# Optimization experiments

Measured on AMD Instinct MI355X. Metric: run time of the kernel, lower is better.

The kernel has to match this reference:

```python
import jax, jax.numpy as jnp
import numpy as np

WH, WW = 12, 12
NUM_HEADS = 8
NW = 4


def _relative_position_index():
    ch, cw = np.meshgrid(np.arange(WH), np.arange(WW), indexing='ij')
    coords = np.stack([ch, cw]).reshape(2, -1)            # [2, Wh*Ww]
    rel = coords[:, :, None] - coords[:, None, :]         # [2, M, M]
    rel = rel.transpose(1, 2, 0)                          # [M, M, 2]
    rel[:, :, 0] += WH - 1
    rel[:, :, 1] += WW - 1
    rel[:, :, 0] *= 2 * WW - 1
    return jnp.asarray(rel.sum(-1))                       # [M, M] int


def setup_inputs() -> dict:
    key = jax.random.key(0)
    ks = jax.random.split(key, 11)
    C = 512
    B_, N = 512, WH * WW + 1
    std = 0.02
    return {
        'x': jax.random.normal(ks[0], (B_, N, C), dtype=jnp.float32),
        'mask': jnp.zeros((NW, N, N), dtype=jnp.float32),
        'rpb_table': jax.random.normal(ks[1], ((2 * WH - 1) * (2 * WW - 1), NUM_HEADS), dtype=jnp.float32) * std,
        'Wq': jax.random.normal(ks[2], (C, C), dtype=jnp.float32) * (C ** -0.5),
        'bq': jax.random.normal(ks[3], (C,), dtype=jnp.float32) * std,
        'Wk': jax.random.normal(ks[4], (C, C), dtype=jnp.float32) * (C ** -0.5),
        'bk': jax.random.normal(ks[5], (C,), dtype=jnp.float32) * std,
        'Wv': jax.random.normal(ks[6], (C, C), dtype=jnp.float32) * (C ** -0.5),
        'bv': jax.random.normal(ks[7], (C,), dtype=jnp.float32) * std,
        'Wo': jax.random.normal(ks[8], (C, C), dtype=jnp.float32) * (C ** -0.5),
        'bo': jax.random.normal(ks[9], (C,), dtype=jnp.float32) * std,
    }


def reference(x, mask, rpb_table, Wq, bq, Wk, bk, Wv, bv, Wo, bo):
    B_, N, C = x.shape
    H = NUM_HEADS
    hd = C // H
    scale = hd ** -0.5
    B = B_ // NW
    M = WH * WW  # window tokens (N = M + 1 global token)

    def proj(W, b):
        return (x @ W.T + b).reshape(B_, N, H, hd).transpose(0, 2, 1, 3)  # [B_,H,N,hd]

    q = proj(Wq, bq)
    k = proj(Wk, bk)
    v = proj(Wv, bv)

    attn = jnp.einsum('bhnd,bhmd->bhnm', q, k) * scale  # [B_,H,N,N]

    rel_idx = _relative_position_index()                 # [M,M]
    bias = rpb_table[rel_idx].transpose(2, 0, 1)          # [H,M,M]
    attn = attn.at[:, :, :M, :M].add(bias[None])          # N != M: bias on window block only

    # shifted-window mask: (nW, N, N)
    attn = (attn.reshape(B, NW, H, N, N) + mask[None, :, None]).reshape(B_, H, N, N)

    # ---- global-token attention redistribution (gx) ----
    ga = attn[:, :, -1, :].reshape(B, NW, H, N).transpose(0, 2, 1, 3)   # [B,H,NW,N]
    g1 = ga[:, :, :, :M].reshape(B, H, NW * M)                           # window keys, all windows
    g2 = ga[:, :, :, M].mean(-1, keepdims=True)                          # mean global-global logit [B,H,1]
    g = jax.nn.softmax(jnp.concatenate([g1, g2], axis=-1), axis=-1)      # [B,H,NW*M+1]
    g1 = g[:, :, :-1].reshape(B, H, NW, M).transpose(0, 2, 1, 3).reshape(B_, H, M)
    g2 = jnp.broadcast_to(g[:, :, -1][:, None, :], (B, NW, H)).reshape(B_, H, 1)
    ga_full = jnp.concatenate([g1, g2], axis=-1)[:, :, None, :]          # [B_,H,1,N]
    gx = jnp.einsum('bhqn,bhnd->bhqd', ga_full, v).transpose(0, 2, 1, 3).reshape(B_, C)
    gx = gx.reshape(B, NW, C).sum(1)                                     # sum over windows [B,C]
    gx = jnp.broadcast_to(gx[:, None, :], (B, NW, C)).reshape(B_, C)

    # ---- standard window attention ----
    attn = jax.nn.softmax(attn, axis=-1)
    out = jnp.einsum('bhnm,bhmd->bhnd', attn, v).transpose(0, 2, 1, 3).reshape(B_, N, C)
    out = out.at[:, -1, :].set(gx)
    return out @ Wo.T + bo
```

## Files before the change

kernel.cpp:

```cpp
#include <hip/hip_runtime.h>
#include <hip/hip_bf16.h>
#include <stdint.h>

#define NTOK 145
#define MTOK 144
#define CDIM 512
#define NHEAD 8
#define HD 64
#define NWIN 4
#define BWIN 512
#define MROWS (BWIN*NTOK)

typedef short short8 __attribute__((ext_vector_type(8)));
typedef float f32x4 __attribute__((ext_vector_type(4)));

__device__ __forceinline__ uint16_t f2bf(float f) {
  union { float f; uint32_t u; } x; x.f = f;
  uint32_t r = x.u + 0x7FFFu + ((x.u >> 16) & 1u);
  return (uint16_t)(r >> 16);
}
__device__ __forceinline__ float bf2f(uint16_t u) {
  union { uint32_t u; float f; } x; x.u = ((uint32_t)u) << 16; return x.f;
}
__device__ __forceinline__ uint32_t pack2(float a, float b) {
  return (uint32_t)f2bf(a) | ((uint32_t)f2bf(b) << 16);
}

#define GLL(gp, lp) __builtin_amdgcn_global_load_lds( \
    (const __attribute__((address_space(1))) uint32_t*)(gp), \
    (__attribute__((address_space(3))) uint32_t*)(lp), 16, 0, 0)

__global__ __launch_bounds__(256) void cast_x(const float* __restrict__ x,
                                              uint16_t* __restrict__ xb) {
  size_t id = ((size_t)blockIdx.x*256 + threadIdx.x)*8;
  float4 a = *(const float4*)(x+id), c = *(const float4*)(x+id+4);
  uint4 o = make_uint4(pack2(a.x,a.y), pack2(a.z,a.w), pack2(c.x,c.y), pack2(c.z,c.w));
  *(uint4*)(xb+id) = o;
}

__global__ void prep_kernel(const float* __restrict__ rpb,
                            const float* __restrict__ Wq, const float* __restrict__ bq,
                            const float* __restrict__ Wk, const float* __restrict__ bk,
                            const float* __restrict__ Wv, const float* __restrict__ bv,
                            const float* __restrict__ Wo,
                            uint16_t* __restrict__ wqkv, uint16_t* __restrict__ wo,
                            float* __restrict__ bqkv, float* __restrict__ biastab) {
  int id = blockIdx.x * 256 + threadIdx.x;
  const int A = 1536*512, B = 512*512, C2 = 1536, D = 8*144*144;
  if (id < A) {
    int n = id >> 9, k = id & 511;
    const float* W = (n < 512) ? Wq : (n < 1024) ? Wk : Wv;
    wqkv[id] = f2bf(W[(size_t)(n & 511)*512 + k]);
  } else if ((id -= A) < B) {
    wo[id] = f2bf(Wo[id]);
  } else if ((id -= B) < C2) {
    bqkv[id] = (id < 512) ? bq[id] : (id < 1024) ? bk[id-512] : bv[id-1024];
  } else if ((id -= C2) < D) {
    int h = id / (144*144); int rr = id % (144*144);
    int i = rr / 144, j = rr % 144;
    int rel = (i/12 - j/12 + 11) * 23 + (i%12 - j%12 + 11);
    biastab[id] = rpb[rel*8 + h];
  }
}

__global__ __launch_bounds__(256) void gemm_qkv(
    const uint16_t* __restrict__ xb, const uint16_t* __restrict__ wqkv,
    const float* __restrict__ bqkv,
    uint16_t* __restrict__ qb, uint16_t* __restrict__ kb, uint16_t* __restrict__ vb) {
  __shared__ __align__(16) uint16_t As[128*32];
  __shared__ __align__(16) uint16_t Bs[128*32];
  int bid = blockIdx.x;
  int mb, nb;
  if (bid < 6912) { int g = bid / 96, r = bid % 96; mb = g*8 + (r & 7); nb = r >> 3; }
  else           { int r = bid - 6912;              mb = 576 + (r & 3); nb = r >> 2; }
  int tid = threadIdx.x;
  int lane = tid & 63, w = tid >> 6;
  int wm = w >> 1, wn = w & 1;
  int lm = lane & 15, lq = lane >> 4;

  int srow = lane >> 2, scol = (lane & 3) * 8;
  const uint16_t* agp = xb   + (size_t)(mb*128 + w*32 + srow)*512 + scol;
  const uint16_t* bgp = wqkv + (size_t)(nb*128 + w*32 + srow)*512 + scol;
  uint16_t* Asw = &As[w*32*32];
  uint16_t* Bsw = &Bs[w*32*32];

  f32x4 acc[4][4];
#pragma unroll
  for (int a = 0; a < 4; a++)
#pragma unroll
    for (int b = 0; b < 4; b++) acc[a][b] = (f32x4){0.f,0.f,0.f,0.f};

  for (int kt = 0; kt < 16; kt++) {
    GLL(agp + kt*32,          Asw);
    GLL(agp + kt*32 + 16*512, Asw + 16*32);
    GLL(bgp + kt*32,          Bsw);
    GLL(bgp + kt*32 + 16*512, Bsw + 16*32);
    __syncthreads();
    short8 a[4], b[4];
#pragma unroll
    for (int t = 0; t < 4; t++) a[t] = *(short8*)&As[(wm*64 + t*16 + lm)*32 + lq*8];
#pragma unroll
    for (int t = 0; t < 4; t++) b[t] = *(short8*)&Bs[(wn*64 + t*16 + lm)*32 + lq*8];
#pragma unroll
    for (int tm = 0; tm < 4; tm++)
#pragma unroll
      for (int tn = 0; tn < 4; tn++)
        acc[tm][tn] = __builtin_amdgcn_mfma_f32_16x16x32_bf16(a[tm], b[tn], acc[tm][tn], 0, 0, 0);
    __syncthreads();
  }
#pragma unroll
  for (int tn = 0; tn < 4; tn++) {
    int n = nb*128 + wn*64 + tn*16 + lm;
    float bias = bqkv[n];
    int which = n >> 9, c = n & 511;
    uint16_t* dst = (which == 0) ? qb : (which == 1) ? kb : vb;
    int hh = c >> 6, dd = c & 63;
#pragma unroll
    for (int tm = 0; tm < 4; tm++) {
#pragma unroll
      for (int r = 0; r < 4; r++) {
        int m = mb*128 + wm*64 + tm*16 + lq*4 + r;
        int bw = m / 145, nl = m - bw*145;
        dst[((size_t)(bw*8 + hh)*145 + nl)*64 + dd] = f2bf(acc[tm][tn][r] + bias);
      }
    }
  }
}

__global__ __launch_bounds__(256, 2) void attn_kernel(
    const uint16_t* __restrict__ qb, const uint16_t* __restrict__ kb,
    const uint16_t* __restrict__ vb, const float* __restrict__ biastab,
    const float* __restrict__ mask, float* __restrict__ glog,
    uint16_t* __restrict__ attn_out) {
  __shared__ __align__(16) uint16_t P[144*160];
  __shared__ __align__(16) uint16_t vs[145*64];
  int bid = blockIdx.x;
  int b_ = bid >> 3, h = bid & 7;
  int nw = b_ & 3;
  int tid = threadIdx.x, lane = tid & 63, w = tid >> 6;
  int lm = lane & 15, lq = lane >> 4;
  const size_t hbase = ((size_t)(b_*8 + h)) * (145*64);
  const uint16_t* qp = qb + hbase;
  const uint16_t* kp = kb + hbase;
  const uint16_t* vp = vb + hbase;

  for (int c = tid; c < 1160; c += 256)
    *(uint4*)&vs[c*8] = *(const uint4*)(vp + (size_t)c*8);

  int nmt = (w < 2) ? 3 : 2;
  f32x4 acc[3][10];
#pragma unroll
  for (int a = 0; a < 3; a++)
#pragma unroll
    for (int b = 0; b < 10; b++) acc[a][b] = (f32x4){0.f,0.f,0.f,0.f};

#pragma unroll
  for (int ks = 0; ks < 2; ks++) {
    short8 bfr[10];
#pragma unroll
    for (int nt = 0; nt < 10; nt++) {
      int j = nt*16 + lm; if (j > 144) j = 144;
      bfr[nt] = *(const short8*)(kp + (size_t)j*64 + ks*32 + lq*8);
    }
#pragma unroll
    for (int mtl = 0; mtl < 3; mtl++) {
      if (mtl < nmt) {
        int mt = w + mtl*4;
        int i = mt*16 + lm; if (i > 144) i = 144;
        short8 afr = *(const short8*)(qp + (size_t)i*64 + ks*32 + lq*8);
#pragma unroll
        for (int nt = 0; nt < 10; nt++)
          acc[mtl][nt] = __builtin_amdgcn_mfma_f32_16x16x32_bf16(afr, bfr[nt], acc[mtl][nt], 0, 0, 0);
      }
    }
  }

  const float scale = 0.125f;
#pragma unroll
  for (int mtl = 0; mtl < 3; mtl++) {
    if (mtl >= nmt) continue;
    int mt = w + mtl*4;
    if (mt == 9) {
      if (lq == 0) {
#pragma unroll
        for (int nt = 0; nt < 10; nt++) {
          int j = nt*16 + lm;
          if (j < 145)
            glog[(size_t)(b_*8 + h)*145 + j] =
                acc[mtl][nt][0]*scale + mask[(nw*145 + 144)*145 + j];
        }
      }
      continue;
    }
#pragma unroll
    for (int r = 0; r < 4; r++) {
      int i = mt*16 + lq*4 + r;
      float mx = -3.0e38f;
#pragma unroll
      for (int nt = 0; nt < 10; nt++) {
        int j = nt*16 + lm;
        float t = acc[mtl][nt][r]*scale;
        if (j < 145) t += mask[(nw*145 + i)*145 + j];
        if (j < 144) t += biastab[(h*144 + i)*144 + j];
        if (j >= 145) t = -3.0e38f;
        acc[mtl][nt][r] = t;
        mx = fmaxf(mx, t);
      }
#pragma unroll
      for (int off = 1; off < 16; off <<= 1) mx = fmaxf(mx, __shfl_xor(mx, off));
      float sum = 0.f;
#pragma unroll
      for (int nt = 0; nt < 10; nt++) {
        int j = nt*16 + lm;
        float p = (j < 145) ? __expf(acc[mtl][nt][r] - mx) : 0.f;
        acc[mtl][nt][r] = p; sum += p;
      }
#pragma unroll
      for (int off = 1; off < 16; off <<= 1) sum += __shfl_xor(sum, off);
      float rs = __builtin_amdgcn_rcpf(sum);
#pragma unroll
      for (int nt = 0; nt < 10; nt++)
        P[i*160 + nt*16 + lm] = f2bf(acc[mtl][nt][r] * rs);
    }
  }
  __syncthreads();

  f32x4 oacc[9];
#pragma unroll
  for (int a = 0; a < 9; a++) oacc[a] = (f32x4){0.f,0.f,0.f,0.f};
#pragma unroll
  for (int ks = 0; ks < 5; ks++) {
    short8 bfr;
#pragma unroll
    for (int jj = 0; jj < 8; jj++) {
      int j = ks*32 + lq*8 + jj; if (j > 144) j = 144;
      bfr[jj] = (short)vs[j*64 + w*16 + lm];
    }
#pragma unroll
    for (int mt = 0; mt < 9; mt++) {
      short8 afr = *(short8*)&P[(mt*16 + lm)*160 + ks*32 + lq*8];
      oacc[mt] = __builtin_amdgcn_mfma_f32_16x16x32_bf16(afr, bfr, oacc[mt], 0, 0, 0);
    }
  }
#pragma unroll
  for (int mt = 0; mt < 9; mt++) {
#pragma unroll
    for (int r = 0; r < 4; r++) {
      int i = mt*16 + lq*4 + r;
      attn_out[((size_t)b_*145 + i)*512 + h*64 + w*16 + lm] = f2bf(oacc[mt][r]);
    }
  }
}

__global__ __launch_bounds__(256) void gx_kernel(
    const float* __restrict__ glog, const uint16_t* __restrict__ vb,
    uint16_t* __restrict__ attn_out) {
  int bid = blockIdx.x;
  int b = bid >> 3, h = bid & 7;
  int tid = threadIdx.x, lane = tid & 63, w = tid >> 6;
  __shared__ float lg[580];
  __shared__ float pl[576];
  __shared__ float sred[8];
  __shared__ float sacc[256];
  for (int t = tid; t < 580; t += 256) {
    int nwi = t / 145, j = t - nwi*145;
    lg[t] = glog[(size_t)((b*4 + nwi)*8 + h)*145 + j];
  }
  __syncthreads();
  float g2 = 0.25f*(lg[144] + lg[289] + lg[434] + lg[579]);
  float mx = g2;
  for (int t = tid; t < 576; t += 256) {
    int nwi = t / 144, j = t - nwi*144;
    mx = fmaxf(mx, lg[nwi*145 + j]);
  }
#pragma unroll
  for (int off = 1; off < 64; off <<= 1) mx = fmaxf(mx, __shfl_xor(mx, off));
  if (lane == 0) sred[w] = mx;
  __syncthreads();
  mx = fmaxf(fmaxf(sred[0], sred[1]), fmaxf(sred[2], sred[3]));
  float sum = 0.f;
  for (int t = tid; t < 576; t += 256) {
    int nwi = t / 144, j = t - nwi*144;
    float p = __expf(lg[nwi*145 + j] - mx);
    pl[t] = p; sum += p;
  }
#pragma unroll
  for (int off = 1; off < 64; off <<= 1) sum += __shfl_xor(sum, off);
  if (lane == 0) sred[4 + w] = sum;
  __syncthreads();
  sum = (sred[4] + sred[5]) + (sred[6] + sred[7]);
  float p2 = __expf(g2 - mx);
  float rs = __builtin_amdgcn_rcpf(sum + p2);
  const uint16_t* vp = vb + (size_t)((b*4 + w)*8 + h)*(145*64);
  float acc = 0.f;
  int d = lane;
#pragma unroll 4
  for (int j = 0; j < 144; j++)
    acc += pl[w*144 + j] * bf2f(vp[j*64 + d]);
  acc += p2 * bf2f(vp[144*64 + d]);
  sacc[tid] = acc;
  __syncthreads();
  if (w == 0) {
    float tot = (sacc[lane] + sacc[64 + lane]) + (sacc[128 + lane] + sacc[192 + lane]);
    uint16_t o = f2bf(tot * rs);
    for (int nwi = 0; nwi < 4; nwi++)
      attn_out[((size_t)(b*4 + nwi)*145 + 144)*512 + h*64 + d] = o;
  }
}

__global__ __launch_bounds__(256) void gemm_out(
    const uint16_t* __restrict__ A, const uint16_t* __restrict__ wo,
    const float* __restrict__ bo, float* __restrict__ out) {
  __shared__ __align__(16) uint16_t As[128*32];
  __shared__ __align__(16) uint16_t Bs[128*32];
  int bid = blockIdx.x;
  int mb, nb;
  if (bid < 2304) { int g = bid / 32, r = bid % 32; mb = g*8 + (r & 7); nb = r >> 3; }
  else            { int r = bid - 2304;             mb = 576 + (r & 3); nb = r >> 2; }
  int tid = threadIdx.x;
  int lane = tid & 63, w = tid >> 6;
  int wm = w >> 1, wn = w & 1;
  int lm = lane & 15, lq = lane >> 4;

  int srow = lane >> 2, scol = (lane & 3) * 8;
  const uint16_t* agp = A  + (size_t)(mb*128 + w*32 + srow)*512 + scol;
  const uint16_t* bgp = wo + (size_t)(nb*128 + w*32 + srow)*512 + scol;
  uint16_t* Asw = &As[w*32*32];
  uint16_t* Bsw = &Bs[w*32*32];

  f32x4 acc[4][4];
#pragma unroll
  for (int a = 0; a < 4; a++)
#pragma unroll
    for (int b = 0; b < 4; b++) acc[a][b] = (f32x4){0.f,0.f,0.f,0.f};

  for (int kt = 0; kt < 16; kt++) {
    GLL(agp + kt*32,          Asw);
    GLL(agp + kt*32 + 16*512, Asw + 16*32);
    GLL(bgp + kt*32,          Bsw);
    GLL(bgp + kt*32 + 16*512, Bsw + 16*32);
    __syncthreads();
    short8 a[4], b[4];
#pragma unroll
    for (int t = 0; t < 4; t++) a[t] = *(short8*)&As[(wm*64 + t*16 + lm)*32 + lq*8];
#pragma unroll
    for (int t = 0; t < 4; t++) b[t] = *(short8*)&Bs[(wn*64 + t*16 + lm)*32 + lq*8];
#pragma unroll
    for (int tm = 0; tm < 4; tm++)
#pragma unroll
      for (int tn = 0; tn < 4; tn++)
        acc[tm][tn] = __builtin_amdgcn_mfma_f32_16x16x32_bf16(a[tm], b[tn], acc[tm][tn], 0, 0, 0);
    __syncthreads();
  }
#pragma unroll
  for (int tn = 0; tn < 4; tn++) {
    int n = nb*128 + wn*64 + tn*16 + lm;
    float bias = bo[n];
#pragma unroll
    for (int tm = 0; tm < 4; tm++) {
#pragma unroll
      for (int r = 0; r < 4; r++) {
        int m = mb*128 + wm*64 + tm*16 + lq*4 + r;
        out[(size_t)m*512 + n] = acc[tm][tn][r] + bias;
      }
    }
  }
}

extern "C" void kernel_launch(void* const* d_in, const int* in_sizes, int n_in,
                              void* d_out, int out_size, void* d_ws, size_t ws_size,
                              hipStream_t stream) {
  const float* x    = (const float*)d_in[0];
  const float* mask = (const float*)d_in[1];
  const float* rpb  = (const float*)d_in[2];
  const float* Wq   = (const float*)d_in[3];
  const float* bq   = (const float*)d_in[4];
  const float* Wk   = (const float*)d_in[5];
  const float* bk   = (const float*)d_in[6];
  const float* Wv   = (const float*)d_in[7];
  const float* bv   = (const float*)d_in[8];
  const float* Wo   = (const float*)d_in[9];
  const float* bo   = (const float*)d_in[10];

  uint8_t* ws = (uint8_t*)d_ws;
  size_t off = 0;
  auto alloc = [&](size_t bytes) -> void* {
    void* p = ws + off; off += (bytes + 255) & ~(size_t)255; return p;
  };
  uint16_t* wqkv   = (uint16_t*)alloc((size_t)1536*512*2);
  uint16_t* wo     = (uint16_t*)alloc((size_t)512*512*2);
  float*    bqkv   = (float*)alloc(1536*4);
  float*    biastab= (float*)alloc((size_t)8*144*144*4);
  float*    glog   = (float*)alloc((size_t)512*8*145*4);
  uint16_t* xb     = (uint16_t*)alloc((size_t)MROWS*512*2);
  uint16_t* qb     = (uint16_t*)alloc((size_t)MROWS*512*2);
  uint16_t* kb     = (uint16_t*)alloc((size_t)MROWS*512*2);
  uint16_t* vb     = (uint16_t*)alloc((size_t)MROWS*512*2);
  uint16_t* attn   = (uint16_t*)alloc((size_t)MROWS*512*2);

  cast_x<<<18560, 256, 0, stream>>>(x, xb);
  prep_kernel<<<4750, 256, 0, stream>>>(rpb, Wq, bq, Wk, bk, Wv, bv, Wo,
                                        wqkv, wo, bqkv, biastab);
  gemm_qkv<<<580*12, 256, 0, stream>>>(xb, wqkv, bqkv, qb, kb, vb);
  attn_kernel<<<4096, 256, 0, stream>>>(qb, kb, vb, biastab, mask, glog, attn);
  gx_kernel<<<1024, 256, 0, stream>>>(glog, vb, attn);
  gemm_out<<<580*4, 256, 0, stream>>>(attn, wo, bo, (float*)d_out);
}
```

Measured before the change: 728.3 us.

## Split attention rows across two blocks and pre-fuse mask with position bias

The attention kernel now splits each (window, head) pair into two blocks, each handling about half of the query row tiles. This doubles the grid and shrinks per-block LDS so occupancy can rise to 3 blocks per CU. The mask and relative position bias are merged in prep into one padded logit table, which seeds the QK accumulator (pre-multiplied by 8) so the softmax loop does no extra adds. V is stored transposed in LDS so PV B-fragments come from a single vector load. In exchange, K is reloaded by both halves, the prep table is larger, and the accumulator-seeding trick relies on the scale being exactly 1/8.

Measured after the change: 723.4 us. No clear change (-0.7%).

```diff
diff --git a/kernel.cpp b/kernel.cpp
--- a/kernel.cpp
+++ b/kernel.cpp
@@ -42,11 +42,11 @@
                             const float* __restrict__ Wq, const float* __restrict__ bq,
                             const float* __restrict__ Wk, const float* __restrict__ bk,
                             const float* __restrict__ Wv, const float* __restrict__ bv,
-                            const float* __restrict__ Wo,
+                            const float* __restrict__ Wo, const float* __restrict__ mask,
                             uint16_t* __restrict__ wqkv, uint16_t* __restrict__ wo,
-                            float* __restrict__ bqkv, float* __restrict__ biastab) {
+                            float* __restrict__ bqkv, float* __restrict__ ltab) {
   int id = blockIdx.x * 256 + threadIdx.x;
-  const int A = 1536*512, B = 512*512, C2 = 1536, D = 8*144*144;
+  const int A = 1536*512, B = 512*512, C2 = 1536, E = 4*8*145*160;
   if (id < A) {
     int n = id >> 9, k = id & 511;
     const float* W = (n < 512) ? Wq : (n < 1024) ? Wk : Wv;
@@ -55,11 +55,19 @@
     wo[id] = f2bf(Wo[id]);
   } else if ((id -= B) < C2) {
     bqkv[id] = (id < 512) ? bq[id] : (id < 1024) ? bk[id-512] : bv[id-1024];
-  } else if ((id -= C2) < D) {
-    int h = id / (144*144); int rr = id % (144*144);
-    int i = rr / 144, j = rr % 144;
-    int rel = (i/12 - j/12 + 11) * 23 + (i%12 - j%12 + 11);
-    biastab[id] = rpb[rel*8 + h];
+  } else if ((id -= C2) < E) {
+    int nw = id / (8*145*160);
+    int r2 = id % (8*145*160);
+    int h = r2 / (145*160);
+    int r3 = r2 % (145*160);
+    int i = r3 / 160, j = r3 % 160;
+    float v = 0.f;
+    if (j < 145) v = mask[(nw*145 + i)*145 + j];
+    if (i < 144 && j < 144) {
+      int rel = (i/12 - j/12 + 11) * 23 + (i%12 - j%12 + 11);
+      v += rpb[rel*8 + h];
+    }
+    ltab[id] = v;
   }
 }
 
@@ -127,15 +135,16 @@
   }
 }
 
-__global__ __launch_bounds__(256, 2) void attn_kernel(
+__global__ __launch_bounds__(256, 3) void attn_kernel(
     const uint16_t* __restrict__ qb, const uint16_t* __restrict__ kb,
-    const uint16_t* __restrict__ vb, const float* __restrict__ biastab,
-    const float* __restrict__ mask, float* __restrict__ glog,
-    uint16_t* __restrict__ attn_out) {
-  __shared__ __align__(16) uint16_t P[144*160];
-  __shared__ __align__(16) uint16_t vs[145*64];
+    const uint16_t* __restrict__ vb, const float* __restrict__ ltab,
+    float* __restrict__ glog, uint16_t* __restrict__ attn_out) {
+  __shared__ __align__(16) uint16_t P[80*168];
+  __shared__ __align__(16) uint16_t vt[64*168];
   int bid = blockIdx.x;
-  int b_ = bid >> 3, h = bid & 7;
+  int half = bid & 1;
+  int h = (bid >> 1) & 7;
+  int b_ = bid >> 4;
   int nw = b_ & 3;
   int tid = threadIdx.x, lane = tid & 63, w = tid >> 6;
   int lm = lane & 15, lq = lane >> 4;
@@ -143,111 +152,105 @@
   const uint16_t* qp = qb + hbase;
   const uint16_t* kp = kb + hbase;
   const uint16_t* vp = vb + hbase;
-
-  for (int c = tid; c < 1160; c += 256)
-    *(uint4*)&vs[c*8] = *(const uint4*)(vp + (size_t)c*8);
-
-  int nmt = (w < 2) ? 3 : 2;
-  f32x4 acc[3][10];
-#pragma unroll
-  for (int a = 0; a < 3; a++)
-#pragma unroll
-    for (int b = 0; b < 10; b++) acc[a][b] = (f32x4){0.f,0.f,0.f,0.f};
-
-#pragma unroll
-  for (int ks = 0; ks < 2; ks++) {
-    short8 bfr[10];
+  const float* ltp = ltab + (size_t)(nw*8 + h)*(145*160);
+
+  for (int c = tid; c < 1160; c += 256) {
+    int j = c >> 3, d0 = (c & 7) * 8;
+    uint16_t tmp[8];
+    *(uint4*)tmp = *(const uint4*)(vp + (size_t)j*64 + d0);
+#pragma unroll
+    for (int t = 0; t < 8; t++) vt[(d0 + t)*168 + j] = tmp[t];
+  }
+  for (int c = tid; c < 960; c += 256)
+    vt[(c/15)*168 + 145 + (c%15)] = 0;
+
+  for (int ltile = w; ltile < 5; ltile += 4) {
+    int gt = half*5 + ltile;
+    f32x4 acc[10];
 #pragma unroll
     for (int nt = 0; nt < 10; nt++) {
-      int j = nt*16 + lm; if (j > 144) j = 144;
-      bfr[nt] = *(const short8*)(kp + (size_t)j*64 + ks*32 + lq*8);
-    }
-#pragma unroll
-    for (int mtl = 0; mtl < 3; mtl++) {
-      if (mtl < nmt) {
-        int mt = w + mtl*4;
-        int i = mt*16 + lm; if (i > 144) i = 144;
-        short8 afr = *(const short8*)(qp + (size_t)i*64 + ks*32 + lq*8);
-#pragma unroll
-        for (int nt = 0; nt < 10; nt++)
-          acc[mtl][nt] = __builtin_amdgcn_mfma_f32_16x16x32_bf16(afr, bfr[nt], acc[mtl][nt], 0, 0, 0);
-      }
-    }
-  }
-
-  const float scale = 0.125f;
-#pragma unroll
-  for (int mtl = 0; mtl < 3; mtl++) {
-    if (mtl >= nmt) continue;
-    int mt = w + mtl*4;
-    if (mt == 9) {
+#pragma unroll
+      for (int r = 0; r < 4; r++) {
+        int i = gt*16 + lq*4 + r; if (i > 144) i = 144;
+        acc[nt][r] = 8.0f * ltp[i*160 + nt*16 + lm];
+      }
+    }
+    int iq = gt*16 + lm; if (iq > 144) iq = 144;
+#pragma unroll
+    for (int ks = 0; ks < 2; ks++) {
+      short8 afr = *(const short8*)(qp + (size_t)iq*64 + ks*32 + lq*8);
+#pragma unroll
+      for (int nt = 0; nt < 10; nt++) {
+        int j = nt*16 + lm; if (j > 144) j = 144;
+        short8 bfr = *(const short8*)(kp + (size_t)j*64 + ks*32 + lq*8);
+        acc[nt] = __builtin_amdgcn_mfma_f32_16x16x32_bf16(afr, bfr, acc[nt], 0, 0, 0);
+      }
+    }
+    if (gt == 9) {
       if (lq == 0) {
 #pragma unroll
         for (int nt = 0; nt < 10; nt++) {
           int j = nt*16 + lm;
           if (j < 145)
-            glog[(size_t)(b_*8 + h)*145 + j] =
-                acc[mtl][nt][0]*scale + mask[(nw*145 + 144)*145 + j];
+            glog[(size_t)(b_*8 + h)*145 + j] = acc[nt][0]*0.125f;
         }
       }
-      continue;
-    }
-#pragma unroll
-    for (int r = 0; r < 4; r++) {
-      int i = mt*16 + lq*4 + r;
-      float mx = -3.0e38f;
-#pragma unroll
-      for (int nt = 0; nt < 10; nt++) {
-        int j = nt*16 + lm;
-        float t = acc[mtl][nt][r]*scale;
-        if (j < 145) t += mask[(nw*145 + i)*145 + j];
-        if (j < 144) t += biastab[(h*144 + i)*144 + j];
-        if (j >= 145) t = -3.0e38f;
-        acc[mtl][nt][r] = t;
-        mx = fmaxf(mx, t);
-      }
-#pragma unroll
-      for (int off = 1; off < 16; off <<= 1) mx = fmaxf(mx, __shfl_xor(mx, off));
-      float sum = 0.f;
-#pragma unroll
-      for (int nt = 0; nt < 10; nt++) {
-        int j = nt*16 + lm;
-        float p = (j < 145) ? __expf(acc[mtl][nt][r] - mx) : 0.f;
-        acc[mtl][nt][r] = p; sum += p;
-      }
-#pragma unroll
-      for (int off = 1; off < 16; off <<= 1) sum += __shfl_xor(sum, off);
-      float rs = __builtin_amdgcn_rcpf(sum);
-#pragma unroll
-      for (int nt = 0; nt < 10; nt++)
-        P[i*160 + nt*16 + lm] = f2bf(acc[mtl][nt][r] * rs);
+    } else {
+#pragma unroll
+      for (int r = 0; r < 4; r++) {
+        int prow = ltile*16 + lq*4 + r;
+        float mx = -3.0e38f;
+#pragma unroll
+        for (int nt = 0; nt < 10; nt++) {
+          int j = nt*16 + lm;
+          float t = acc[nt][r]*0.125f;
+          if (j >= 145) t = -3.0e38f;
+          acc[nt][r] = t;
+          mx = fmaxf(mx, t);
+        }
+#pragma unroll
+        for (int off = 1; off < 16; off <<= 1) mx = fmaxf(mx, __shfl_xor(mx, off));
+        float sum = 0.f;
+#pragma unroll
+        for (int nt = 0; nt < 10; nt++) {
+          int j = nt*16 + lm;
+          float p = (j < 145) ? __expf(acc[nt][r] - mx) : 0.f;
+          acc[nt][r] = p; sum += p;
+        }
+#pragma unroll
+        for (int off = 1; off < 16; off <<= 1) sum += __shfl_xor(sum, off);
+        float rs = __builtin_amdgcn_rcpf(sum);
+#pragma unroll
+        for (int nt = 0; nt < 10; nt++)
+          P[prow*168 + nt*16 + lm] = f2bf(acc[nt][r] * rs);
+      }
     }
   }
   __syncthreads();
 
-  f32x4 oacc[9];
-#pragma unroll
-  for (int a = 0; a < 9; a++) oacc[a] = (f32x4){0.f,0.f,0.f,0.f};
+  int npv = 5 - half;
+  f32x4 oacc[5];
+#pragma unroll
+  for (int mt = 0; mt < 5; mt++) oacc[mt] = (f32x4){0.f,0.f,0.f,0.f};
 #pragma unroll
   for (int ks = 0; ks < 5; ks++) {
-    short8 bfr;
-#pragma unroll
-    for (int jj = 0; jj < 8; jj++) {
-      int j = ks*32 + lq*8 + jj; if (j > 144) j = 144;
-      bfr[jj] = (short)vs[j*64 + w*16 + lm];
-    }
-#pragma unroll
-    for (int mt = 0; mt < 9; mt++) {
-      short8 afr = *(short8*)&P[(mt*16 + lm)*160 + ks*32 + lq*8];
-      oacc[mt] = __builtin_amdgcn_mfma_f32_16x16x32_bf16(afr, bfr, oacc[mt], 0, 0, 0);
-    }
-  }
-#pragma unroll
-  for (int mt = 0; mt < 9; mt++) {
-#pragma unroll
-    for (int r = 0; r < 4; r++) {
-      int i = mt*16 + lq*4 + r;
-      attn_out[((size_t)b_*145 + i)*512 + h*64 + w*16 + lm] = f2bf(oacc[mt][r]);
+    short8 bfr = *(const short8*)&vt[(w*16 + lm)*168 + ks*32 + lq*8];
+#pragma unroll
+    for (int mt = 0; mt < 5; mt++) {
+      if (mt < npv) {
+        short8 afr = *(const short8*)&P[(mt*16 + lm)*168 + ks*32 + lq*8];
+        oacc[mt] = __builtin_amdgcn_mfma_f32_16x16x32_bf16(afr, bfr, oacc[mt], 0, 0, 0);
+      }
+    }
+  }
+#pragma unroll
+  for (int mt = 0; mt < 5; mt++) {
+    if (mt < npv) {
+#pragma unroll
+      for (int r = 0; r < 4; r++) {
+        int i = half*80 + mt*16 + lq*4 + r;
+        attn_out[((size_t)b_*145 + i)*512 + h*64 + w*16 + lm] = f2bf(oacc[mt][r]);
+      }
     }
   }
 }
@@ -390,7 +393,7 @@
   uint16_t* wqkv   = (uint16_t*)alloc((size_t)1536*512*2);
   uint16_t* wo     = (uint16_t*)alloc((size_t)512*512*2);
   float*    bqkv   = (float*)alloc(1536*4);
-  float*    biastab= (float*)alloc((size_t)8*144*144*4);
+  float*    ltab   = (float*)alloc((size_t)4*8*145*160*4);
   float*    glog   = (float*)alloc((size_t)512*8*145*4);
   uint16_t* xb     = (uint16_t*)alloc((size_t)MROWS*512*2);
   uint16_t* qb     = (uint16_t*)alloc((size_t)MROWS*512*2);
@@ -399,10 +402,10 @@
   uint16_t* attn   = (uint16_t*)alloc((size_t)MROWS*512*2);
 
   cast_x<<<18560, 256, 0, stream>>>(x, xb);
-  prep_kernel<<<4750, 256, 0, stream>>>(rpb, Wq, bq, Wk, bk, Wv, bv, Wo,
-                                        wqkv, wo, bqkv, biastab);
+  prep_kernel<<<7002, 256, 0, stream>>>(rpb, Wq, bq, Wk, bk, Wv, bv, Wo, mask,
+                                        wqkv, wo, bqkv, ltab);
   gemm_qkv<<<580*12, 256, 0, stream>>>(xb, wqkv, bqkv, qb, kb, vb);
-  attn_kernel<<<4096, 256, 0, stream>>>(qb, kb, vb, biastab, mask, glog, attn);
+  attn_kernel<<<8192, 256, 0, stream>>>(qb, kb, vb, ltab, glog, attn);
   gx_kernel<<<1024, 256, 0, stream>>>(glog, vb, attn);
   gemm_out<<<580*4, 256, 0, stream>>>(attn, wo, bo, (float*)d_out);
 }
```
